# Kernel optimization log

Measured on AMD Instinct MI355X. Metric: run time of the kernel, lower is better.

The kernel has to match this reference:

```python
import jax, jax.numpy as jnp
import numpy as np

LN_EPS = 1e-5
Q_EPS = 1e-5


def ternary_quantize(w):
    # BitNet b1.58-style: scale by mean(|W|), round, clip to {-1, 0, 1}
    scale = jnp.mean(jnp.abs(w))
    return jnp.clip(jnp.round(w / (scale + Q_EPS)), -1.0, 1.0)


def layernorm(x, gamma, beta):
    mu = jnp.mean(x, axis=-1, keepdims=True)
    var = jnp.mean(jnp.square(x - mu), axis=-1, keepdims=True)
    return (x - mu) * jax.lax.rsqrt(var + LN_EPS) * gamma + beta


def setup_inputs() -> dict:
    key = jax.random.key(0)
    k_x, k_w = jax.random.split(key)
    B, S, D_IN, D_OUT = 4, 2048, 2048, 2048
    x = jax.random.normal(k_x, (B, S, D_IN), dtype=jnp.float32)
    # kaiming_normal_ fan_out, relu: std = sqrt(2 / fan_out) = sqrt(2 / out_features)
    std = np.sqrt(2.0 / D_OUT).astype(np.float32)
    weight = jax.random.normal(k_w, (D_OUT, D_IN), dtype=jnp.float32) * std
    bias = jnp.zeros((D_OUT,), dtype=jnp.float32)
    ln_gamma = jnp.ones((D_IN,), dtype=jnp.float32)
    ln_beta = jnp.zeros((D_IN,), dtype=jnp.float32)
    return {"x": x, "weight": weight, "bias": bias, "ln_gamma": ln_gamma, "ln_beta": ln_beta}


def reference(x, weight, bias, ln_gamma, ln_beta):
    xn = layernorm(x, ln_gamma, ln_beta)          # [B, S, D_in]
    w_q = ternary_quantize(weight)                 # [D_out, D_in] in {-1, 0, 1}
    return jnp.einsum('bsi,oi->bso', xn, w_q) + bias
```

## Files before the change

kernel.cpp:

```cpp
#include <hip/hip_runtime.h>
#include <hip/hip_bf16.h>

#define D_IN  2048
#define D_OUT 2048
#define M_TOTAL 8192

typedef __attribute__((ext_vector_type(4))) int   i32x4;
typedef __attribute__((ext_vector_type(4))) float f32x4;

typedef const __attribute__((address_space(1))) void gvoid_t;
typedef __attribute__((address_space(3))) void lvoid_t;

__global__ __launch_bounds__(256) void absum_kernel(const float* __restrict__ w,
                                                    double* __restrict__ partials) {
    const int n4 = (D_OUT * D_IN) / 4;
    int tid = blockIdx.x * 256 + threadIdx.x;
    int stride = gridDim.x * 256;
    double s = 0.0;
    for (int i = tid; i < n4; i += stride) {
        float4 v = reinterpret_cast<const float4*>(w)[i];
        s += (double)fabsf(v.x) + (double)fabsf(v.y) +
             (double)fabsf(v.z) + (double)fabsf(v.w);
    }
    for (int off = 32; off; off >>= 1) s += __shfl_xor(s, off, 64);
    __shared__ double ls[4];
    if ((threadIdx.x & 63) == 0) ls[threadIdx.x >> 6] = s;
    __syncthreads();
    if (threadIdx.x == 0)
        partials[blockIdx.x] = ls[0] + ls[1] + ls[2] + ls[3];
}

__global__ __launch_bounds__(256) void quant_kernel(const float* __restrict__ w,
                                                    const double* __restrict__ partials,
                                                    char* __restrict__ wq) {
    int t = threadIdx.x;
    double s = partials[t] + partials[t + 256] + partials[t + 512] + partials[t + 768];
    for (int off = 32; off; off >>= 1) s += __shfl_xor(s, off, 64);
    __shared__ double ls[4];
    if ((t & 63) == 0) ls[t >> 6] = s;
    __syncthreads();
    double tot = ls[0] + ls[1] + ls[2] + ls[3];
    double inv = 1.0 / (tot / 4194304.0 + 1e-5);

    int i = blockIdx.x * 256 + t;
    float4 v = reinterpret_cast<const float4*>(w)[i];
    unsigned o = 0;
    #pragma unroll
    for (int j = 0; j < 4; ++j) {
        float wf = (j == 0) ? v.x : (j == 1) ? v.y : (j == 2) ? v.z : v.w;
        double r = rint((double)wf * inv);
        r = fmin(1.0, fmax(-1.0, r));
        int q = (int)r;
        o |= ((unsigned)(unsigned char)(char)q) << (8 * j);
    }
    reinterpret_cast<unsigned*>(wq)[i] = o;
}

__device__ __forceinline__ unsigned pk4(float a, float b, float c, float d, float is) {
    int q0 = (int)rintf(a * is); q0 = min(127, max(-127, q0));
    int q1 = (int)rintf(b * is); q1 = min(127, max(-127, q1));
    int q2 = (int)rintf(c * is); q2 = min(127, max(-127, q2));
    int q3 = (int)rintf(d * is); q3 = min(127, max(-127, q3));
    return  (unsigned)(unsigned char)(char)q0        |
           ((unsigned)(unsigned char)(char)q1 << 8)  |
           ((unsigned)(unsigned char)(char)q2 << 16) |
           ((unsigned)(unsigned char)(char)q3 << 24);
}

__global__ __launch_bounds__(256) void ln_kernel(const float* __restrict__ x,
                                                 const float* __restrict__ gamma,
                                                 const float* __restrict__ beta,
                                                 char* __restrict__ xn,
                                                 float* __restrict__ s_row) {
    int row = blockIdx.x;
    const float4* xr = reinterpret_cast<const float4*>(x + (size_t)row * D_IN);
    int t = threadIdx.x;
    float4 v0 = xr[t];
    float4 v1 = xr[t + 256];
    float s  = v0.x + v0.y + v0.z + v0.w + v1.x + v1.y + v1.z + v1.w;
    float sq = v0.x*v0.x + v0.y*v0.y + v0.z*v0.z + v0.w*v0.w
             + v1.x*v1.x + v1.y*v1.y + v1.z*v1.z + v1.w*v1.w;
    for (int off = 32; off; off >>= 1) {
        s  += __shfl_xor(s,  off, 64);
        sq += __shfl_xor(sq, off, 64);
    }
    __shared__ float lss[4], lqq[4], lmx[4];
    if ((t & 63) == 0) { lss[t >> 6] = s; lqq[t >> 6] = sq; }
    __syncthreads();
    s  = lss[0] + lss[1] + lss[2] + lss[3];
    sq = lqq[0] + lqq[1] + lqq[2] + lqq[3];
    float mu  = s * (1.0f / D_IN);
    float var = sq * (1.0f / D_IN) - mu * mu;
    float inv = rsqrtf(var + 1e-5f);

    const float4* g4 = reinterpret_cast<const float4*>(gamma);
    const float4* b4 = reinterpret_cast<const float4*>(beta);
    float4 g0 = g4[t], g1 = g4[t + 256];
    float4 b0 = b4[t], b1 = b4[t + 256];

    float a0 = (v0.x - mu) * inv * g0.x + b0.x;
    float a1 = (v0.y - mu) * inv * g0.y + b0.y;
    float a2 = (v0.z - mu) * inv * g0.z + b0.z;
    float a3 = (v0.w - mu) * inv * g0.w + b0.w;
    float a4 = (v1.x - mu) * inv * g1.x + b1.x;
    float a5 = (v1.y - mu) * inv * g1.y + b1.y;
    float a6 = (v1.z - mu) * inv * g1.z + b1.z;
    float a7 = (v1.w - mu) * inv * g1.w + b1.w;

    float mx = fmaxf(fmaxf(fmaxf(fabsf(a0), fabsf(a1)), fmaxf(fabsf(a2), fabsf(a3))),
                     fmaxf(fmaxf(fabsf(a4), fabsf(a5)), fmaxf(fabsf(a6), fabsf(a7))));
    for (int off = 32; off; off >>= 1) mx = fmaxf(mx, __shfl_xor(mx, off, 64));
    if ((t & 63) == 0) lmx[t >> 6] = mx;
    __syncthreads();
    float rowmax = fmaxf(fmaxf(lmx[0], lmx[1]), fmaxf(lmx[2], lmx[3]));

    float is = (rowmax > 0.0f) ? (127.0f / rowmax) : 0.0f;
    char* orow = xn + (size_t)row * D_IN;
    reinterpret_cast<unsigned*>(orow)[t]        = pk4(a0, a1, a2, a3, is);
    reinterpret_cast<unsigned*>(orow + 1024)[t] = pk4(a4, a5, a6, a7, is);
    if (t == 0) s_row[row] = rowmax * (1.0f / 127.0f);
}

#define BM 256
#define BN 256
#define NT (D_IN / 64)

__device__ __forceinline__ void stage_quantum(const char* __restrict__ gbase,
                                              int grow0, int kcol0,
                                              char* smem, int ldsbase, int tid) {
    const int lane = tid & 63;
    const int w    = tid >> 6;
    const int colx = (((lane & 3) ^ ((lane >> 3) & 3)) << 4);
    #pragma unroll
    for (int j = 0; j < 2; ++j) {
        const int c = w * 2 + j;
        const int r = c * 16 + (lane >> 2);
        const char* g = gbase + (size_t)(grow0 + r) * D_IN + kcol0 + colx;
        char* l = smem + ldsbase + c * 1024 + lane * 16;
        __builtin_amdgcn_global_load_lds((gvoid_t*)g, (lvoid_t*)l, 16, 0, 0);
    }
}

__device__ __forceinline__ i32x4 rdfrag(const char* smem, int off) {
    return *reinterpret_cast<const i32x4*>(smem + off);
}

template<int W>
__device__ __forceinline__ void vm_wait() {
    if constexpr (W == 4) {
        asm volatile("s_waitcnt vmcnt(4)" ::: "memory");
        __builtin_amdgcn_sched_barrier(0);
    } else if constexpr (W == 0) {
        asm volatile("s_waitcnt vmcnt(0)" ::: "memory");
        __builtin_amdgcn_sched_barrier(0);
    }
}

#define MFMA16(ROW, AV, BV)                                                     \
    __builtin_amdgcn_sched_barrier(0);                                          \
    __builtin_amdgcn_s_setprio(1);                                              \
    _Pragma("unroll")                                                           \
    for (int m_ = 0; m_ < 4; ++m_)                                              \
        _Pragma("unroll")                                                       \
        for (int n_ = 0; n_ < 4; ++n_)                                          \
            acc[ROW + m_][n_] = __builtin_amdgcn_mfma_i32_16x16x64_i8(          \
                AV[m_], BV[n_], acc[ROW + m_][n_], 0, 0, 0);                    \
    __builtin_amdgcn_s_setprio(0);                                              \
    __builtin_amdgcn_sched_barrier(0);

template<int W, bool S, bool RD>
__device__ __forceinline__ void ktile(int T,
        const char* __restrict__ A, const char* __restrict__ B,
        int bm, int bn, char* smem, int tid, int aBase, int bBase,
        i32x4 (&aS0)[4], i32x4 (&aS1)[4], i32x4 (&bCur)[4], i32x4 (&bNxt)[4],
        i32x4 (&acc)[8][4]) {
    const int sA  = ((T & 3) << 14);
    const int sAn = (((T + 1) & 3) << 14);

    #pragma unroll
    for (int f = 0; f < 4; ++f) aS1[f] = rdfrag(smem, sA + aBase + 4096 + f * 1024);
    MFMA16(0, aS0, bCur)
    vm_wait<W>();
    __builtin_amdgcn_s_barrier();

    if (RD) {
        #pragma unroll
        for (int f = 0; f < 4; ++f) aS0[f]  = rdfrag(smem, sAn + aBase + f * 1024);
        #pragma unroll
        for (int f = 0; f < 4; ++f) bNxt[f] = rdfrag(smem, 65536 + sAn + bBase + f * 1024);
    }
    if (S) {
        const int s3 = (((T + 3) & 3) << 14);
        stage_quantum(A, bm, (T + 3) * 64, smem, s3,         tid);
        stage_quantum(B, bn, (T + 3) * 64, smem, 65536 + s3, tid);
    }
    MFMA16(4, aS1, bCur)
    __builtin_amdgcn_s_barrier();
}

__global__ __launch_bounds__(512, 2) void gemm256_kernel(const char* __restrict__ A,
                                                         const char* __restrict__ B,
                                                         const float* __restrict__ bias,
                                                         const float* __restrict__ s_row,
                                                         float* __restrict__ C) {
    extern __shared__ char smem[];
    const int tid  = threadIdx.x;
    const int lane = tid & 63;
    const int wid  = tid >> 6;
    const int wm   = wid >> 2;
    const int wn   = wid & 3;

    const int orig = blockIdx.y * gridDim.x + blockIdx.x;
    const int swz  = (orig & 7) * 32 + (orig >> 3);
    const int bm   = (swz >> 3) * BM;
    const int bn   = (swz & 7) * BN;

    const int lr   = lane & 15;
    const int rdbase = lr * 64 + ((((lane >> 4) ^ ((lr >> 1) & 3))) << 4);
    const int aBase = wm * 8192 + rdbase;
    const int bBase = wn * 4096 + rdbase;

    i32x4 acc[8][4];
    #pragma unroll
    for (int m = 0; m < 8; ++m)
        #pragma unroll
        for (int n = 0; n < 4; ++n)
            acc[m][n] = (i32x4){0, 0, 0, 0};

    i32x4 aS0[4], aS1[4], bE[4], bO[4];

    stage_quantum(A, bm, 0,   smem, 0,             tid);
    stage_quantum(B, bn, 0,   smem, 65536,         tid);
    stage_quantum(A, bm, 64,  smem, 16384,         tid);
    stage_quantum(B, bn, 64,  smem, 65536 + 16384, tid);
    stage_quantum(A, bm, 128, smem, 32768,         tid);
    stage_quantum(B, bn, 128, smem, 65536 + 32768, tid);
    asm volatile("s_waitcnt vmcnt(8)" ::: "memory");
    __builtin_amdgcn_sched_barrier(0);
    __builtin_amdgcn_s_barrier();
    #pragma unroll
    for (int f = 0; f < 4; ++f) aS0[f] = rdfrag(smem, aBase + f * 1024);
    #pragma unroll
    for (int f = 0; f < 4; ++f) bE[f]  = rdfrag(smem, 65536 + bBase + f * 1024);
    __builtin_amdgcn_sched_barrier(0);

    for (int T = 0; T < 28; T += 2) {
        ktile<4, true, true>(T,     A, B, bm, bn, smem, tid, aBase, bBase, aS0, aS1, bE, bO, acc);
        ktile<4, true, true>(T + 1, A, B, bm, bn, smem, tid, aBase, bBase, aS0, aS1, bO, bE, acc);
    }
    ktile<4,  true,  true >(28, A, B, bm, bn, smem, tid, aBase, bBase, aS0, aS1, bE, bO, acc);
    ktile<4,  false, true >(29, A, B, bm, bn, smem, tid, aBase, bBase, aS0, aS1, bO, bE, acc);
    ktile<0,  false, true >(30, A, B, bm, bn, smem, tid, aBase, bBase, aS0, aS1, bE, bO, acc);
    ktile<-1, false, false>(31, A, B, bm, bn, smem, tid, aBase, bBase, aS0, aS1, bO, bE, acc);

    const int EST = 272;
    char* eb = smem + wid * (16 * EST);
    const int C0 = bn + wn * 64;
    const int R0 = bm + wm * 128;
    const int rowsub = (lane >> 4) * 4;
    float bv[4];
    #pragma unroll
    for (int n = 0; n < 4; ++n) bv[n] = bias[C0 + n * 16 + lr];

    #pragma unroll
    for (int m = 0; m < 8; ++m) {
        float sr[4];
        #pragma unroll
        for (int i = 0; i < 4; ++i) sr[i] = s_row[R0 + m * 16 + rowsub + i];
        #pragma unroll
        for (int n = 0; n < 4; ++n)
            #pragma unroll
            for (int i = 0; i < 4; ++i)
                *reinterpret_cast<float*>(eb + (rowsub + i) * EST + (n * 16 + lr) * 4)
                    = (float)acc[m][n][i] * sr[i] + bv[n];
        #pragma unroll
        for (int q = 0; q < 4; ++q) {
            const int row = (lane >> 4) + q * 4;
            f32x4 v = *reinterpret_cast<const f32x4*>(eb + row * EST + lr * 16);
            *reinterpret_cast<f32x4*>(&C[(size_t)(R0 + m * 16 + row) * D_OUT + C0 + lr * 4]) = v;
        }
    }
}

extern "C" void kernel_launch(void* const* d_in, const int* in_sizes, int n_in,
                              void* d_out, int out_size, void* d_ws, size_t ws_size,
                              hipStream_t stream) {
    const float* x     = (const float*)d_in[0];
    const float* w     = (const float*)d_in[1];
    const float* bias  = (const float*)d_in[2];
    const float* gamma = (const float*)d_in[3];
    const float* beta  = (const float*)d_in[4];
    float* out = (float*)d_out;

    char* ws = (char*)d_ws;
    double* partials = (double*)ws;
    float*  s_row    = (float*)(ws + 8192);
    char*   wq       = ws + 65536;
    char*   xn       = ws + 65536 + 4ull * 1024 * 1024;

    hipFuncSetAttribute(reinterpret_cast<const void*>(gemm256_kernel),
                        hipFuncAttributeMaxDynamicSharedMemorySize, 131072);

    absum_kernel   <<<1024, 256, 0, stream>>>(w, partials);
    quant_kernel   <<<4096, 256, 0, stream>>>(w, partials, wq);
    ln_kernel      <<<M_TOTAL, 256, 0, stream>>>(x, gamma, beta, xn, s_row);
    gemm256_kernel <<<dim3(D_OUT / BN, M_TOTAL / BM), 512, 131072, stream>>>(xn, wq, bias, s_row, out);
}
```

Measured before the change: 70.00 us.

## Merge quant and layernorm kernels; shrink GEMM tile to 256x128 with double buffering

Combines the weight-quantization and layernorm kernels into one launch that picks its branch from the block index, removing one kernel launch. The int8 GEMM moves from a 256x256 tile with 512 threads, a 4-deep dynamic-LDS pipeline and register prefetch to a 256x128 tile with 256 threads and a two-slot static LDS double buffer. Loads for the next k-tile are issued in the middle of the MFMA work. The smaller tile doubles the block count and lowers LDS use so two blocks can share a CU, at the cost of less data reuse per tile and a shallower prefetch that waits on vmcnt(0) every tile.

```diff
diff --git a/kernel.cpp b/kernel.cpp
--- a/kernel.cpp
+++ b/kernel.cpp
@@ -30,32 +30,6 @@
         partials[blockIdx.x] = ls[0] + ls[1] + ls[2] + ls[3];
 }
 
-__global__ __launch_bounds__(256) void quant_kernel(const float* __restrict__ w,
-                                                    const double* __restrict__ partials,
-                                                    char* __restrict__ wq) {
-    int t = threadIdx.x;
-    double s = partials[t] + partials[t + 256] + partials[t + 512] + partials[t + 768];
-    for (int off = 32; off; off >>= 1) s += __shfl_xor(s, off, 64);
-    __shared__ double ls[4];
-    if ((t & 63) == 0) ls[t >> 6] = s;
-    __syncthreads();
-    double tot = ls[0] + ls[1] + ls[2] + ls[3];
-    double inv = 1.0 / (tot / 4194304.0 + 1e-5);
-
-    int i = blockIdx.x * 256 + t;
-    float4 v = reinterpret_cast<const float4*>(w)[i];
-    unsigned o = 0;
-    #pragma unroll
-    for (int j = 0; j < 4; ++j) {
-        float wf = (j == 0) ? v.x : (j == 1) ? v.y : (j == 2) ? v.z : v.w;
-        double r = rint((double)wf * inv);
-        r = fmin(1.0, fmax(-1.0, r));
-        int q = (int)r;
-        o |= ((unsigned)(unsigned char)(char)q) << (8 * j);
-    }
-    reinterpret_cast<unsigned*>(wq)[i] = o;
-}
-
 __device__ __forceinline__ unsigned pk4(float a, float b, float c, float d, float is) {
     int q0 = (int)rintf(a * is); q0 = min(127, max(-127, q0));
     int q1 = (int)rintf(b * is); q1 = min(127, max(-127, q1));
@@ -67,73 +41,98 @@
            ((unsigned)(unsigned char)(char)q3 << 24);
 }
 
-__global__ __launch_bounds__(256) void ln_kernel(const float* __restrict__ x,
-                                                 const float* __restrict__ gamma,
-                                                 const float* __restrict__ beta,
-                                                 char* __restrict__ xn,
-                                                 float* __restrict__ s_row) {
-    int row = blockIdx.x;
-    const float4* xr = reinterpret_cast<const float4*>(x + (size_t)row * D_IN);
+__global__ __launch_bounds__(256) void quantln_kernel(const float* __restrict__ w,
+                                                      const double* __restrict__ partials,
+                                                      char* __restrict__ wq,
+                                                      const float* __restrict__ x,
+                                                      const float* __restrict__ gamma,
+                                                      const float* __restrict__ beta,
+                                                      char* __restrict__ xn,
+                                                      float* __restrict__ s_row) {
     int t = threadIdx.x;
-    float4 v0 = xr[t];
-    float4 v1 = xr[t + 256];
-    float s  = v0.x + v0.y + v0.z + v0.w + v1.x + v1.y + v1.z + v1.w;
-    float sq = v0.x*v0.x + v0.y*v0.y + v0.z*v0.z + v0.w*v0.w
-             + v1.x*v1.x + v1.y*v1.y + v1.z*v1.z + v1.w*v1.w;
-    for (int off = 32; off; off >>= 1) {
-        s  += __shfl_xor(s,  off, 64);
-        sq += __shfl_xor(sq, off, 64);
-    }
-    __shared__ float lss[4], lqq[4], lmx[4];
-    if ((t & 63) == 0) { lss[t >> 6] = s; lqq[t >> 6] = sq; }
-    __syncthreads();
-    s  = lss[0] + lss[1] + lss[2] + lss[3];
-    sq = lqq[0] + lqq[1] + lqq[2] + lqq[3];
-    float mu  = s * (1.0f / D_IN);
-    float var = sq * (1.0f / D_IN) - mu * mu;
-    float inv = rsqrtf(var + 1e-5f);
-
-    const float4* g4 = reinterpret_cast<const float4*>(gamma);
-    const float4* b4 = reinterpret_cast<const float4*>(beta);
-    float4 g0 = g4[t], g1 = g4[t + 256];
-    float4 b0 = b4[t], b1 = b4[t + 256];
-
-    float a0 = (v0.x - mu) * inv * g0.x + b0.x;
-    float a1 = (v0.y - mu) * inv * g0.y + b0.y;
-    float a2 = (v0.z - mu) * inv * g0.z + b0.z;
-    float a3 = (v0.w - mu) * inv * g0.w + b0.w;
-    float a4 = (v1.x - mu) * inv * g1.x + b1.x;
-    float a5 = (v1.y - mu) * inv * g1.y + b1.y;
-    float a6 = (v1.z - mu) * inv * g1.z + b1.z;
-    float a7 = (v1.w - mu) * inv * g1.w + b1.w;
-
-    float mx = fmaxf(fmaxf(fmaxf(fabsf(a0), fabsf(a1)), fmaxf(fabsf(a2), fabsf(a3))),
-                     fmaxf(fmaxf(fabsf(a4), fabsf(a5)), fmaxf(fabsf(a6), fabsf(a7))));
-    for (int off = 32; off; off >>= 1) mx = fmaxf(mx, __shfl_xor(mx, off, 64));
-    if ((t & 63) == 0) lmx[t >> 6] = mx;
-    __syncthreads();
-    float rowmax = fmaxf(fmaxf(lmx[0], lmx[1]), fmaxf(lmx[2], lmx[3]));
-
-    float is = (rowmax > 0.0f) ? (127.0f / rowmax) : 0.0f;
-    char* orow = xn + (size_t)row * D_IN;
-    reinterpret_cast<unsigned*>(orow)[t]        = pk4(a0, a1, a2, a3, is);
-    reinterpret_cast<unsigned*>(orow + 1024)[t] = pk4(a4, a5, a6, a7, is);
-    if (t == 0) s_row[row] = rowmax * (1.0f / 127.0f);
-}
-
-#define BM 256
-#define BN 256
+    if (blockIdx.x < 4096) {
+        double s = partials[t] + partials[t + 256] + partials[t + 512] + partials[t + 768];
+        for (int off = 32; off; off >>= 1) s += __shfl_xor(s, off, 64);
+        __shared__ double ls[4];
+        if ((t & 63) == 0) ls[t >> 6] = s;
+        __syncthreads();
+        double tot = ls[0] + ls[1] + ls[2] + ls[3];
+        double inv = 1.0 / (tot / 4194304.0 + 1e-5);
+
+        int i = blockIdx.x * 256 + t;
+        float4 v = reinterpret_cast<const float4*>(w)[i];
+        unsigned o = 0;
+        #pragma unroll
+        for (int j = 0; j < 4; ++j) {
+            float wf = (j == 0) ? v.x : (j == 1) ? v.y : (j == 2) ? v.z : v.w;
+            double r = rint((double)wf * inv);
+            r = fmin(1.0, fmax(-1.0, r));
+            int q = (int)r;
+            o |= ((unsigned)(unsigned char)(char)q) << (8 * j);
+        }
+        reinterpret_cast<unsigned*>(wq)[i] = o;
+    } else {
+        int row = blockIdx.x - 4096;
+        const float4* xr = reinterpret_cast<const float4*>(x + (size_t)row * D_IN);
+        float4 v0 = xr[t];
+        float4 v1 = xr[t + 256];
+        float s  = v0.x + v0.y + v0.z + v0.w + v1.x + v1.y + v1.z + v1.w;
+        float sq = v0.x*v0.x + v0.y*v0.y + v0.z*v0.z + v0.w*v0.w
+                 + v1.x*v1.x + v1.y*v1.y + v1.z*v1.z + v1.w*v1.w;
+        for (int off = 32; off; off >>= 1) {
+            s  += __shfl_xor(s,  off, 64);
+            sq += __shfl_xor(sq, off, 64);
+        }
+        __shared__ float lss[4], lqq[4], lmx[4];
+        if ((t & 63) == 0) { lss[t >> 6] = s; lqq[t >> 6] = sq; }
+        __syncthreads();
+        s  = lss[0] + lss[1] + lss[2] + lss[3];
+        sq = lqq[0] + lqq[1] + lqq[2] + lqq[3];
+        float mu  = s * (1.0f / D_IN);
+        float var = sq * (1.0f / D_IN) - mu * mu;
+        float inv = rsqrtf(var + 1e-5f);
+
+        const float4* g4 = reinterpret_cast<const float4*>(gamma);
+        const float4* b4 = reinterpret_cast<const float4*>(beta);
+        float4 g0 = g4[t], g1 = g4[t + 256];
+        float4 b0 = b4[t], b1 = b4[t + 256];
+
+        float a0 = (v0.x - mu) * inv * g0.x + b0.x;
+        float a1 = (v0.y - mu) * inv * g0.y + b0.y;
+        float a2 = (v0.z - mu) * inv * g0.z + b0.z;
+        float a3 = (v0.w - mu) * inv * g0.w + b0.w;
+        float a4 = (v1.x - mu) * inv * g1.x + b1.x;
+        float a5 = (v1.y - mu) * inv * g1.y + b1.y;
+        float a6 = (v1.z - mu) * inv * g1.z + b1.z;
+        float a7 = (v1.w - mu) * inv * g1.w + b1.w;
+
+        float mx = fmaxf(fmaxf(fmaxf(fabsf(a0), fabsf(a1)), fmaxf(fabsf(a2), fabsf(a3))),
+                         fmaxf(fmaxf(fabsf(a4), fabsf(a5)), fmaxf(fabsf(a6), fabsf(a7))));
+        for (int off = 32; off; off >>= 1) mx = fmaxf(mx, __shfl_xor(mx, off, 64));
+        if ((t & 63) == 0) lmx[t >> 6] = mx;
+        __syncthreads();
+        float rowmax = fmaxf(fmaxf(lmx[0], lmx[1]), fmaxf(lmx[2], lmx[3]));
+
+        float is = (rowmax > 0.0f) ? (127.0f / rowmax) : 0.0f;
+        char* orow = xn + (size_t)row * D_IN;
+        reinterpret_cast<unsigned*>(orow)[t]        = pk4(a0, a1, a2, a3, is);
+        reinterpret_cast<unsigned*>(orow + 1024)[t] = pk4(a4, a5, a6, a7, is);
+        if (t == 0) s_row[row] = rowmax * (1.0f / 127.0f);
+    }
+}
+
 #define NT (D_IN / 64)
-
-__device__ __forceinline__ void stage_quantum(const char* __restrict__ gbase,
-                                              int grow0, int kcol0,
-                                              char* smem, int ldsbase, int tid) {
+#define SLOT2 24576
+
+__device__ __forceinline__ void stageA(const char* __restrict__ gbase,
+                                       int grow0, int kcol0,
+                                       char* smem, int ldsbase, int tid) {
     const int lane = tid & 63;
     const int w    = tid >> 6;
     const int colx = (((lane & 3) ^ ((lane >> 3) & 3)) << 4);
     #pragma unroll
-    for (int j = 0; j < 2; ++j) {
-        const int c = w * 2 + j;
+    for (int j = 0; j < 4; ++j) {
+        const int c = j * 4 + w;
         const int r = c * 16 + (lane >> 2);
         const char* g = gbase + (size_t)(grow0 + r) * D_IN + kcol0 + colx;
         char* l = smem + ldsbase + c * 1024 + lane * 16;
@@ -141,16 +140,29 @@
     }
 }
 
+__device__ __forceinline__ void stageB(const char* __restrict__ gbase,
+                                       int grow0, int kcol0,
+                                       char* smem, int ldsbase, int tid) {
+    const int lane = tid & 63;
+    const int w    = tid >> 6;
+    const int colx = (((lane & 3) ^ ((lane >> 3) & 3)) << 4);
+    #pragma unroll
+    for (int j = 0; j < 2; ++j) {
+        const int c = j * 4 + w;
+        const int r = c * 16 + (lane >> 2);
+        const char* g = gbase + (size_t)(grow0 + r) * D_IN + kcol0 + colx;
+        char* l = smem + ldsbase + c * 1024 + lane * 16;
+        __builtin_amdgcn_global_load_lds((gvoid_t*)g, (lvoid_t*)l, 16, 0, 0);
+    }
+}
+
 __device__ __forceinline__ i32x4 rdfrag(const char* smem, int off) {
     return *reinterpret_cast<const i32x4*>(smem + off);
 }
 
 template<int W>
 __device__ __forceinline__ void vm_wait() {
-    if constexpr (W == 4) {
-        asm volatile("s_waitcnt vmcnt(4)" ::: "memory");
-        __builtin_amdgcn_sched_barrier(0);
-    } else if constexpr (W == 0) {
+    if constexpr (W == 0) {
         asm volatile("s_waitcnt vmcnt(0)" ::: "memory");
         __builtin_amdgcn_sched_barrier(0);
     }
@@ -168,52 +180,47 @@
     __builtin_amdgcn_s_setprio(0);                                              \
     __builtin_amdgcn_sched_barrier(0);
 
-template<int W, bool S, bool RD>
+template<bool S, int W>
 __device__ __forceinline__ void ktile(int T,
         const char* __restrict__ A, const char* __restrict__ B,
         int bm, int bn, char* smem, int tid, int aBase, int bBase,
-        i32x4 (&aS0)[4], i32x4 (&aS1)[4], i32x4 (&bCur)[4], i32x4 (&bNxt)[4],
         i32x4 (&acc)[8][4]) {
-    const int sA  = ((T & 3) << 14);
-    const int sAn = (((T + 1) & 3) << 14);
-
-    #pragma unroll
-    for (int f = 0; f < 4; ++f) aS1[f] = rdfrag(smem, sA + aBase + 4096 + f * 1024);
-    MFMA16(0, aS0, bCur)
+    const int sb = (T & 1) * SLOT2;
+    const int so = sb ^ SLOT2;
+
+    i32x4 a0[4], b0[4], a1[4];
+    #pragma unroll
+    for (int f = 0; f < 4; ++f) a0[f] = rdfrag(smem, sb + aBase + f * 1024);
+    #pragma unroll
+    for (int f = 0; f < 4; ++f) b0[f] = rdfrag(smem, sb + 16384 + bBase + f * 1024);
+    if (S) stageA(A, bm, (T + 1) * 64, smem, so, tid);
+    MFMA16(0, a0, b0)
+    __builtin_amdgcn_s_barrier();
+
+    #pragma unroll
+    for (int f = 0; f < 4; ++f) a1[f] = rdfrag(smem, sb + aBase + 4096 + f * 1024);
+    if (S) stageB(B, bn, (T + 1) * 64, smem, so + 16384, tid);
+    MFMA16(4, a1, b0)
     vm_wait<W>();
     __builtin_amdgcn_s_barrier();
-
-    if (RD) {
-        #pragma unroll
-        for (int f = 0; f < 4; ++f) aS0[f]  = rdfrag(smem, sAn + aBase + f * 1024);
-        #pragma unroll
-        for (int f = 0; f < 4; ++f) bNxt[f] = rdfrag(smem, 65536 + sAn + bBase + f * 1024);
-    }
-    if (S) {
-        const int s3 = (((T + 3) & 3) << 14);
-        stage_quantum(A, bm, (T + 3) * 64, smem, s3,         tid);
-        stage_quantum(B, bn, (T + 3) * 64, smem, 65536 + s3, tid);
-    }
-    MFMA16(4, aS1, bCur)
-    __builtin_amdgcn_s_barrier();
-}
-
-__global__ __launch_bounds__(512, 2) void gemm256_kernel(const char* __restrict__ A,
+}
+
+__global__ __launch_bounds__(256, 2) void gemm128_kernel(const char* __restrict__ A,
                                                          const char* __restrict__ B,
                                                          const float* __restrict__ bias,
                                                          const float* __restrict__ s_row,
                                                          float* __restrict__ C) {
-    extern __shared__ char smem[];
+    __shared__ char smem[2 * SLOT2];
     const int tid  = threadIdx.x;
     const int lane = tid & 63;
     const int wid  = tid >> 6;
-    const int wm   = wid >> 2;
-    const int wn   = wid & 3;
+    const int wm   = wid >> 1;
+    const int wn   = wid & 1;
 
     const int orig = blockIdx.y * gridDim.x + blockIdx.x;
-    const int swz  = (orig & 7) * 32 + (orig >> 3);
-    const int bm   = (swz >> 3) * BM;
-    const int bn   = (swz & 7) * BN;
+    const int swz  = (orig & 7) * 64 + (orig >> 3);
+    const int bm   = (swz >> 4) * 256;
+    const int bn   = (swz & 15) * 128;
 
     const int lr   = lane & 15;
     const int rdbase = lr * 64 + ((((lane >> 4) ^ ((lr >> 1) & 3))) << 4);
@@ -227,31 +234,15 @@
         for (int n = 0; n < 4; ++n)
             acc[m][n] = (i32x4){0, 0, 0, 0};
 
-    i32x4 aS0[4], aS1[4], bE[4], bO[4];
-
-    stage_quantum(A, bm, 0,   smem, 0,             tid);
-    stage_quantum(B, bn, 0,   smem, 65536,         tid);
-    stage_quantum(A, bm, 64,  smem, 16384,         tid);
-    stage_quantum(B, bn, 64,  smem, 65536 + 16384, tid);
-    stage_quantum(A, bm, 128, smem, 32768,         tid);
-    stage_quantum(B, bn, 128, smem, 65536 + 32768, tid);
-    asm volatile("s_waitcnt vmcnt(8)" ::: "memory");
+    stageA(A, bm, 0, smem, 0,     tid);
+    stageB(B, bn, 0, smem, 16384, tid);
+    asm volatile("s_waitcnt vmcnt(0)" ::: "memory");
     __builtin_amdgcn_sched_barrier(0);
     __builtin_amdgcn_s_barrier();
-    #pragma unroll
-    for (int f = 0; f < 4; ++f) aS0[f] = rdfrag(smem, aBase + f * 1024);
-    #pragma unroll
-    for (int f = 0; f < 4; ++f) bE[f]  = rdfrag(smem, 65536 + bBase + f * 1024);
-    __builtin_amdgcn_sched_barrier(0);
-
-    for (int T = 0; T < 28; T += 2) {
-        ktile<4, true, true>(T,     A, B, bm, bn, smem, tid, aBase, bBase, aS0, aS1, bE, bO, acc);
-        ktile<4, true, true>(T + 1, A, B, bm, bn, smem, tid, aBase, bBase, aS0, aS1, bO, bE, acc);
-    }
-    ktile<4,  true,  true >(28, A, B, bm, bn, smem, tid, aBase, bBase, aS0, aS1, bE, bO, acc);
-    ktile<4,  false, true >(29, A, B, bm, bn, smem, tid, aBase, bBase, aS0, aS1, bO, bE, acc);
-    ktile<0,  false, true >(30, A, B, bm, bn, smem, tid, aBase, bBase, aS0, aS1, bE, bO, acc);
-    ktile<-1, false, false>(31, A, B, bm, bn, smem, tid, aBase, bBase, aS0, aS1, bO, bE, acc);
+
+    for (int T = 0; T < NT - 1; ++T)
+        ktile<true, 0>(T, A, B, bm, bn, smem, tid, aBase, bBase, acc);
+    ktile<false, -1>(NT - 1, A, B, bm, bn, smem, tid, aBase, bBase, acc);
 
     const int EST = 272;
     char* eb = smem + wid * (16 * EST);
@@ -298,11 +289,7 @@
     char*   wq       = ws + 65536;
     char*   xn       = ws + 65536 + 4ull * 1024 * 1024;
 
-    hipFuncSetAttribute(reinterpret_cast<const void*>(gemm256_kernel),
-                        hipFuncAttributeMaxDynamicSharedMemorySize, 131072);
-
     absum_kernel   <<<1024, 256, 0, stream>>>(w, partials);
-    quant_kernel   <<<4096, 256, 0, stream>>>(w, partials, wq);
-    ln_kernel      <<<M_TOTAL, 256, 0, stream>>>(x, gamma, beta, xn, s_row);
-    gemm256_kernel <<<dim3(D_OUT / BN, M_TOTAL / BM), 512, 131072, stream>>>(xn, wq, bias, s_row, out);
-}
+    quantln_kernel <<<12288, 256, 0, stream>>>(w, partials, wq, x, gamma, beta, xn, s_row);
+    gemm128_kernel <<<dim3(16, 32), 256, 0, stream>>>(xn, wq, bias, s_row, out);
+}
```

Measured after the change: 68.34 us. -2.4%, faster.

## Merge weight-quant and layernorm kernels; use 4-wave GEMM with 128x128 warp tiles

Applied to the files above, without the earlier changes.

The weight quantization and layernorm-quantize kernels become one launch, with the block index deciding which job a block does. This removes one launch and lets the two independent jobs overlap. The GEMM goes from 8 waves per 256x256 block to 4 waves, each computing a 128x128 sub-tile with 64 accumulator vectors. Each wave now issues twice as many async LDS loads and reads twice as many B fragments. This raises register reuse per wave but reduces the number of waves available to hide latency, and puts heavy pressure on the VGPR/AGPR budget.

```diff
diff --git a/kernel.cpp b/kernel.cpp
--- a/kernel.cpp
+++ b/kernel.cpp
@@ -30,32 +30,6 @@
         partials[blockIdx.x] = ls[0] + ls[1] + ls[2] + ls[3];
 }
 
-__global__ __launch_bounds__(256) void quant_kernel(const float* __restrict__ w,
-                                                    const double* __restrict__ partials,
-                                                    char* __restrict__ wq) {
-    int t = threadIdx.x;
-    double s = partials[t] + partials[t + 256] + partials[t + 512] + partials[t + 768];
-    for (int off = 32; off; off >>= 1) s += __shfl_xor(s, off, 64);
-    __shared__ double ls[4];
-    if ((t & 63) == 0) ls[t >> 6] = s;
-    __syncthreads();
-    double tot = ls[0] + ls[1] + ls[2] + ls[3];
-    double inv = 1.0 / (tot / 4194304.0 + 1e-5);
-
-    int i = blockIdx.x * 256 + t;
-    float4 v = reinterpret_cast<const float4*>(w)[i];
-    unsigned o = 0;
-    #pragma unroll
-    for (int j = 0; j < 4; ++j) {
-        float wf = (j == 0) ? v.x : (j == 1) ? v.y : (j == 2) ? v.z : v.w;
-        double r = rint((double)wf * inv);
-        r = fmin(1.0, fmax(-1.0, r));
-        int q = (int)r;
-        o |= ((unsigned)(unsigned char)(char)q) << (8 * j);
-    }
-    reinterpret_cast<unsigned*>(wq)[i] = o;
-}
-
 __device__ __forceinline__ unsigned pk4(float a, float b, float c, float d, float is) {
     int q0 = (int)rintf(a * is); q0 = min(127, max(-127, q0));
     int q1 = (int)rintf(b * is); q1 = min(127, max(-127, q1));
@@ -67,62 +41,86 @@
            ((unsigned)(unsigned char)(char)q3 << 24);
 }
 
-__global__ __launch_bounds__(256) void ln_kernel(const float* __restrict__ x,
-                                                 const float* __restrict__ gamma,
-                                                 const float* __restrict__ beta,
-                                                 char* __restrict__ xn,
-                                                 float* __restrict__ s_row) {
-    int row = blockIdx.x;
-    const float4* xr = reinterpret_cast<const float4*>(x + (size_t)row * D_IN);
+__global__ __launch_bounds__(256) void quantln_kernel(const float* __restrict__ w,
+                                                      const double* __restrict__ partials,
+                                                      char* __restrict__ wq,
+                                                      const float* __restrict__ x,
+                                                      const float* __restrict__ gamma,
+                                                      const float* __restrict__ beta,
+                                                      char* __restrict__ xn,
+                                                      float* __restrict__ s_row) {
     int t = threadIdx.x;
-    float4 v0 = xr[t];
-    float4 v1 = xr[t + 256];
-    float s  = v0.x + v0.y + v0.z + v0.w + v1.x + v1.y + v1.z + v1.w;
-    float sq = v0.x*v0.x + v0.y*v0.y + v0.z*v0.z + v0.w*v0.w
-             + v1.x*v1.x + v1.y*v1.y + v1.z*v1.z + v1.w*v1.w;
-    for (int off = 32; off; off >>= 1) {
-        s  += __shfl_xor(s,  off, 64);
-        sq += __shfl_xor(sq, off, 64);
-    }
-    __shared__ float lss[4], lqq[4], lmx[4];
-    if ((t & 63) == 0) { lss[t >> 6] = s; lqq[t >> 6] = sq; }
-    __syncthreads();
-    s  = lss[0] + lss[1] + lss[2] + lss[3];
-    sq = lqq[0] + lqq[1] + lqq[2] + lqq[3];
-    float mu  = s * (1.0f / D_IN);
-    float var = sq * (1.0f / D_IN) - mu * mu;
-    float inv = rsqrtf(var + 1e-5f);
-
-    const float4* g4 = reinterpret_cast<const float4*>(gamma);
-    const float4* b4 = reinterpret_cast<const float4*>(beta);
-    float4 g0 = g4[t], g1 = g4[t + 256];
-    float4 b0 = b4[t], b1 = b4[t + 256];
-
-    float a0 = (v0.x - mu) * inv * g0.x + b0.x;
-    float a1 = (v0.y - mu) * inv * g0.y + b0.y;
-    float a2 = (v0.z - mu) * inv * g0.z + b0.z;
-    float a3 = (v0.w - mu) * inv * g0.w + b0.w;
-    float a4 = (v1.x - mu) * inv * g1.x + b1.x;
-    float a5 = (v1.y - mu) * inv * g1.y + b1.y;
-    float a6 = (v1.z - mu) * inv * g1.z + b1.z;
-    float a7 = (v1.w - mu) * inv * g1.w + b1.w;
-
-    float mx = fmaxf(fmaxf(fmaxf(fabsf(a0), fabsf(a1)), fmaxf(fabsf(a2), fabsf(a3))),
-                     fmaxf(fmaxf(fabsf(a4), fabsf(a5)), fmaxf(fabsf(a6), fabsf(a7))));
-    for (int off = 32; off; off >>= 1) mx = fmaxf(mx, __shfl_xor(mx, off, 64));
-    if ((t & 63) == 0) lmx[t >> 6] = mx;
-    __syncthreads();
-    float rowmax = fmaxf(fmaxf(lmx[0], lmx[1]), fmaxf(lmx[2], lmx[3]));
-
-    float is = (rowmax > 0.0f) ? (127.0f / rowmax) : 0.0f;
-    char* orow = xn + (size_t)row * D_IN;
-    reinterpret_cast<unsigned*>(orow)[t]        = pk4(a0, a1, a2, a3, is);
-    reinterpret_cast<unsigned*>(orow + 1024)[t] = pk4(a4, a5, a6, a7, is);
-    if (t == 0) s_row[row] = rowmax * (1.0f / 127.0f);
-}
-
-#define BM 256
-#define BN 256
+    if (blockIdx.x < 4096) {
+        double s = partials[t] + partials[t + 256] + partials[t + 512] + partials[t + 768];
+        for (int off = 32; off; off >>= 1) s += __shfl_xor(s, off, 64);
+        __shared__ double ls[4];
+        if ((t & 63) == 0) ls[t >> 6] = s;
+        __syncthreads();
+        double tot = ls[0] + ls[1] + ls[2] + ls[3];
+        double inv = 1.0 / (tot / 4194304.0 + 1e-5);
+
+        int i = blockIdx.x * 256 + t;
+        float4 v = reinterpret_cast<const float4*>(w)[i];
+        unsigned o = 0;
+        #pragma unroll
+        for (int j = 0; j < 4; ++j) {
+            float wf = (j == 0) ? v.x : (j == 1) ? v.y : (j == 2) ? v.z : v.w;
+            double r = rint((double)wf * inv);
+            r = fmin(1.0, fmax(-1.0, r));
+            int q = (int)r;
+            o |= ((unsigned)(unsigned char)(char)q) << (8 * j);
+        }
+        reinterpret_cast<unsigned*>(wq)[i] = o;
+    } else {
+        int row = blockIdx.x - 4096;
+        const float4* xr = reinterpret_cast<const float4*>(x + (size_t)row * D_IN);
+        float4 v0 = xr[t];
+        float4 v1 = xr[t + 256];
+        float s  = v0.x + v0.y + v0.z + v0.w + v1.x + v1.y + v1.z + v1.w;
+        float sq = v0.x*v0.x + v0.y*v0.y + v0.z*v0.z + v0.w*v0.w
+                 + v1.x*v1.x + v1.y*v1.y + v1.z*v1.z + v1.w*v1.w;
+        for (int off = 32; off; off >>= 1) {
+            s  += __shfl_xor(s,  off, 64);
+            sq += __shfl_xor(sq, off, 64);
+        }
+        __shared__ float lss[4], lqq[4], lmx[4];
+        if ((t & 63) == 0) { lss[t >> 6] = s; lqq[t >> 6] = sq; }
+        __syncthreads();
+        s  = lss[0] + lss[1] + lss[2] + lss[3];
+        sq = lqq[0] + lqq[1] + lqq[2] + lqq[3];
+        float mu  = s * (1.0f / D_IN);
+        float var = sq * (1.0f / D_IN) - mu * mu;
+        float inv = rsqrtf(var + 1e-5f);
+
+        const float4* g4 = reinterpret_cast<const float4*>(gamma);
+        const float4* b4 = reinterpret_cast<const float4*>(beta);
+        float4 g0 = g4[t], g1 = g4[t + 256];
+        float4 b0 = b4[t], b1 = b4[t + 256];
+
+        float a0 = (v0.x - mu) * inv * g0.x + b0.x;
+        float a1 = (v0.y - mu) * inv * g0.y + b0.y;
+        float a2 = (v0.z - mu) * inv * g0.z + b0.z;
+        float a3 = (v0.w - mu) * inv * g0.w + b0.w;
+        float a4 = (v1.x - mu) * inv * g1.x + b1.x;
+        float a5 = (v1.y - mu) * inv * g1.y + b1.y;
+        float a6 = (v1.z - mu) * inv * g1.z + b1.z;
+        float a7 = (v1.w - mu) * inv * g1.w + b1.w;
+
+        float mx = fmaxf(fmaxf(fmaxf(fabsf(a0), fabsf(a1)), fmaxf(fabsf(a2), fabsf(a3))),
+                         fmaxf(fmaxf(fabsf(a4), fabsf(a5)), fmaxf(fabsf(a6), fabsf(a7))));
+        for (int off = 32; off; off >>= 1) mx = fmaxf(mx, __shfl_xor(mx, off, 64));
+        if ((t & 63) == 0) lmx[t >> 6] = mx;
+        __syncthreads();
+        float rowmax = fmaxf(fmaxf(lmx[0], lmx[1]), fmaxf(lmx[2], lmx[3]));
+
+        float is = (rowmax > 0.0f) ? (127.0f / rowmax) : 0.0f;
+        char* orow = xn + (size_t)row * D_IN;
+        reinterpret_cast<unsigned*>(orow)[t]        = pk4(a0, a1, a2, a3, is);
+        reinterpret_cast<unsigned*>(orow + 1024)[t] = pk4(a4, a5, a6, a7, is);
+        if (t == 0) s_row[row] = rowmax * (1.0f / 127.0f);
+    }
+}
+
 #define NT (D_IN / 64)
 
 __device__ __forceinline__ void stage_quantum(const char* __restrict__ gbase,
@@ -132,8 +130,8 @@
     const int w    = tid >> 6;
     const int colx = (((lane & 3) ^ ((lane >> 3) & 3)) << 4);
     #pragma unroll
-    for (int j = 0; j < 2; ++j) {
-        const int c = w * 2 + j;
+    for (int j = 0; j < 4; ++j) {
+        const int c = w * 4 + j;
         const int r = c * 16 + (lane >> 2);
         const char* g = gbase + (size_t)(grow0 + r) * D_IN + kcol0 + colx;
         char* l = smem + ldsbase + c * 1024 + lane * 16;
@@ -147,8 +145,8 @@
 
 template<int W>
 __device__ __forceinline__ void vm_wait() {
-    if constexpr (W == 4) {
-        asm volatile("s_waitcnt vmcnt(4)" ::: "memory");
+    if constexpr (W == 8) {
+        asm volatile("s_waitcnt vmcnt(8)" ::: "memory");
         __builtin_amdgcn_sched_barrier(0);
     } else if constexpr (W == 0) {
         asm volatile("s_waitcnt vmcnt(0)" ::: "memory");
@@ -156,13 +154,13 @@
     }
 }
 
-#define MFMA16(ROW, AV, BV)                                                     \
+#define MFMA32(ROW, AV, BV)                                                     \
     __builtin_amdgcn_sched_barrier(0);                                          \
     __builtin_amdgcn_s_setprio(1);                                              \
     _Pragma("unroll")                                                           \
     for (int m_ = 0; m_ < 4; ++m_)                                              \
         _Pragma("unroll")                                                       \
-        for (int n_ = 0; n_ < 4; ++n_)                                          \
+        for (int n_ = 0; n_ < 8; ++n_)                                          \
             acc[ROW + m_][n_] = __builtin_amdgcn_mfma_i32_16x16x64_i8(          \
                 AV[m_], BV[n_], acc[ROW + m_][n_], 0, 0, 0);                    \
     __builtin_amdgcn_s_setprio(0);                                              \
@@ -172,14 +170,14 @@
 __device__ __forceinline__ void ktile(int T,
         const char* __restrict__ A, const char* __restrict__ B,
         int bm, int bn, char* smem, int tid, int aBase, int bBase,
-        i32x4 (&aS0)[4], i32x4 (&aS1)[4], i32x4 (&bCur)[4], i32x4 (&bNxt)[4],
-        i32x4 (&acc)[8][4]) {
+        i32x4 (&aS0)[4], i32x4 (&aS1)[4], i32x4 (&bCur)[8], i32x4 (&bNxt)[8],
+        i32x4 (&acc)[8][8]) {
     const int sA  = ((T & 3) << 14);
     const int sAn = (((T + 1) & 3) << 14);
 
     #pragma unroll
     for (int f = 0; f < 4; ++f) aS1[f] = rdfrag(smem, sA + aBase + 4096 + f * 1024);
-    MFMA16(0, aS0, bCur)
+    MFMA32(0, aS0, bCur)
     vm_wait<W>();
     __builtin_amdgcn_s_barrier();
 
@@ -187,18 +185,18 @@
         #pragma unroll
         for (int f = 0; f < 4; ++f) aS0[f]  = rdfrag(smem, sAn + aBase + f * 1024);
         #pragma unroll
-        for (int f = 0; f < 4; ++f) bNxt[f] = rdfrag(smem, 65536 + sAn + bBase + f * 1024);
+        for (int f = 0; f < 8; ++f) bNxt[f] = rdfrag(smem, 65536 + sAn + bBase + f * 1024);
     }
     if (S) {
         const int s3 = (((T + 3) & 3) << 14);
         stage_quantum(A, bm, (T + 3) * 64, smem, s3,         tid);
         stage_quantum(B, bn, (T + 3) * 64, smem, 65536 + s3, tid);
     }
-    MFMA16(4, aS1, bCur)
+    MFMA32(4, aS1, bCur)
     __builtin_amdgcn_s_barrier();
 }
 
-__global__ __launch_bounds__(512, 2) void gemm256_kernel(const char* __restrict__ A,
+__global__ __launch_bounds__(256, 1) void gemm256_kernel(const char* __restrict__ A,
                                                          const char* __restrict__ B,
                                                          const float* __restrict__ bias,
                                                          const float* __restrict__ s_row,
@@ -207,27 +205,27 @@
     const int tid  = threadIdx.x;
     const int lane = tid & 63;
     const int wid  = tid >> 6;
-    const int wm   = wid >> 2;
-    const int wn   = wid & 3;
+    const int wm   = wid >> 1;
+    const int wn   = wid & 1;
 
     const int orig = blockIdx.y * gridDim.x + blockIdx.x;
     const int swz  = (orig & 7) * 32 + (orig >> 3);
-    const int bm   = (swz >> 3) * BM;
-    const int bn   = (swz & 7) * BN;
+    const int bm   = (swz >> 3) * 256;
+    const int bn   = (swz & 7) * 256;
 
     const int lr   = lane & 15;
     const int rdbase = lr * 64 + ((((lane >> 4) ^ ((lr >> 1) & 3))) << 4);
     const int aBase = wm * 8192 + rdbase;
-    const int bBase = wn * 4096 + rdbase;
-
-    i32x4 acc[8][4];
+    const int bBase = wn * 8192 + rdbase;
+
+    i32x4 acc[8][8];
     #pragma unroll
     for (int m = 0; m < 8; ++m)
         #pragma unroll
-        for (int n = 0; n < 4; ++n)
+        for (int n = 0; n < 8; ++n)
             acc[m][n] = (i32x4){0, 0, 0, 0};
 
-    i32x4 aS0[4], aS1[4], bE[4], bO[4];
+    i32x4 aS0[4], aS1[4], bE[8], bO[8];
 
     stage_quantum(A, bm, 0,   smem, 0,             tid);
     stage_quantum(B, bn, 0,   smem, 65536,         tid);
@@ -235,32 +233,32 @@
     stage_quantum(B, bn, 64,  smem, 65536 + 16384, tid);
     stage_quantum(A, bm, 128, smem, 32768,         tid);
     stage_quantum(B, bn, 128, smem, 65536 + 32768, tid);
-    asm volatile("s_waitcnt vmcnt(8)" ::: "memory");
+    asm volatile("s_waitcnt vmcnt(16)" ::: "memory");
     __builtin_amdgcn_sched_barrier(0);
     __builtin_amdgcn_s_barrier();
     #pragma unroll
     for (int f = 0; f < 4; ++f) aS0[f] = rdfrag(smem, aBase + f * 1024);
     #pragma unroll
-    for (int f = 0; f < 4; ++f) bE[f]  = rdfrag(smem, 65536 + bBase + f * 1024);
+    for (int f = 0; f < 8; ++f) bE[f]  = rdfrag(smem, 65536 + bBase + f * 1024);
     __builtin_amdgcn_sched_barrier(0);
 
     for (int T = 0; T < 28; T += 2) {
-        ktile<4, true, true>(T,     A, B, bm, bn, smem, tid, aBase, bBase, aS0, aS1, bE, bO, acc);
-        ktile<4, true, true>(T + 1, A, B, bm, bn, smem, tid, aBase, bBase, aS0, aS1, bO, bE, acc);
-    }
-    ktile<4,  true,  true >(28, A, B, bm, bn, smem, tid, aBase, bBase, aS0, aS1, bE, bO, acc);
-    ktile<4,  false, true >(29, A, B, bm, bn, smem, tid, aBase, bBase, aS0, aS1, bO, bE, acc);
+        ktile<8, true, true>(T,     A, B, bm, bn, smem, tid, aBase, bBase, aS0, aS1, bE, bO, acc);
+        ktile<8, true, true>(T + 1, A, B, bm, bn, smem, tid, aBase, bBase, aS0, aS1, bO, bE, acc);
+    }
+    ktile<8,  true,  true >(28, A, B, bm, bn, smem, tid, aBase, bBase, aS0, aS1, bE, bO, acc);
+    ktile<8,  false, true >(29, A, B, bm, bn, smem, tid, aBase, bBase, aS0, aS1, bO, bE, acc);
     ktile<0,  false, true >(30, A, B, bm, bn, smem, tid, aBase, bBase, aS0, aS1, bE, bO, acc);
     ktile<-1, false, false>(31, A, B, bm, bn, smem, tid, aBase, bBase, aS0, aS1, bO, bE, acc);
 
-    const int EST = 272;
+    const int EST = 528;
     char* eb = smem + wid * (16 * EST);
-    const int C0 = bn + wn * 64;
+    const int C0 = bn + wn * 128;
     const int R0 = bm + wm * 128;
     const int rowsub = (lane >> 4) * 4;
-    float bv[4];
-    #pragma unroll
-    for (int n = 0; n < 4; ++n) bv[n] = bias[C0 + n * 16 + lr];
+    float bv[8];
+    #pragma unroll
+    for (int n = 0; n < 8; ++n) bv[n] = bias[C0 + n * 16 + lr];
 
     #pragma unroll
     for (int m = 0; m < 8; ++m) {
@@ -268,16 +266,17 @@
         #pragma unroll
         for (int i = 0; i < 4; ++i) sr[i] = s_row[R0 + m * 16 + rowsub + i];
         #pragma unroll
-        for (int n = 0; n < 4; ++n)
+        for (int n = 0; n < 8; ++n)
             #pragma unroll
             for (int i = 0; i < 4; ++i)
                 *reinterpret_cast<float*>(eb + (rowsub + i) * EST + (n * 16 + lr) * 4)
                     = (float)acc[m][n][i] * sr[i] + bv[n];
         #pragma unroll
-        for (int q = 0; q < 4; ++q) {
-            const int row = (lane >> 4) + q * 4;
-            f32x4 v = *reinterpret_cast<const f32x4*>(eb + row * EST + lr * 16);
-            *reinterpret_cast<f32x4*>(&C[(size_t)(R0 + m * 16 + row) * D_OUT + C0 + lr * 4]) = v;
+        for (int q = 0; q < 8; ++q) {
+            const int row = q * 2 + (lane >> 5);
+            const int col = (lane & 31) * 4;
+            f32x4 v = *reinterpret_cast<const f32x4*>(eb + row * EST + col * 4);
+            *reinterpret_cast<f32x4*>(&C[(size_t)(R0 + m * 16 + row) * D_OUT + C0 + col]) = v;
         }
     }
 }
@@ -302,7 +301,6 @@
                         hipFuncAttributeMaxDynamicSharedMemorySize, 131072);
 
     absum_kernel   <<<1024, 256, 0, stream>>>(w, partials);
-    quant_kernel   <<<4096, 256, 0, stream>>>(w, partials, wq);
-    ln_kernel      <<<M_TOTAL, 256, 0, stream>>>(x, gamma, beta, xn, s_row);
-    gemm256_kernel <<<dim3(D_OUT / BN, M_TOTAL / BM), 512, 131072, stream>>>(xn, wq, bias, s_row, out);
-}
+    quantln_kernel <<<12288, 256, 0, stream>>>(w, partials, wq, x, gamma, beta, xn, s_row);
+    gemm256_kernel <<<dim3(8, 32), 256, 131072, stream>>>(xn, wq, bias, s_row, out);
+}
```

Result: no change. 69.73 us (-0.4%).
